# Optimization experiments

Hardware: AMD Instinct MI355X
Metric: run time of the kernel (lower is better)

## Reference

```python
import jax, jax.numpy as jnp
import numpy as np

N_NODES = 50000
N_EDGES = 800000
IN_DIM = 128
HIDDEN = 128
N_CLASSES = 10
BN_EPS = 1e-5


def _sage_conv(x, src, dst, n, w_l, b_l, w_r):
    # PyG SAGEConv (mean aggr): out = lin_l(mean_{j->i} x_j) + lin_r(x_i)
    msg = x[src]  # [E, d] gather
    s = jax.ops.segment_sum(msg, dst, num_segments=n)
    cnt = jax.ops.segment_sum(jnp.ones((src.shape[0], 1), x.dtype), dst, num_segments=n)
    mean = s / jnp.maximum(cnt, 1.0)
    return mean @ w_l.T + b_l + x @ w_r.T


def _bn_eval(x, gamma, beta, mean, var):
    return (x - mean) * (gamma * jax.lax.rsqrt(var + BN_EPS)) + beta


def setup_inputs() -> dict:
    key = jax.random.key(0)
    ks = jax.random.split(key, 16)
    h2 = HIDDEN // 2

    def lin(k, fan_out, fan_in):
        bound = 1.0 / np.sqrt(fan_in)
        return jax.random.uniform(k, (fan_out, fan_in), jnp.float32, -bound, bound)

    return {
        "x": jax.random.normal(ks[0], (N_NODES, IN_DIM), jnp.float32),
        "edge_index": jax.random.randint(ks[1], (2, N_EDGES), 0, N_NODES, jnp.int64),
        "w1l": lin(ks[2], HIDDEN, IN_DIM),
        "b1l": jnp.zeros((HIDDEN,), jnp.float32),
        "w1r": lin(ks[3], HIDDEN, IN_DIM),
        "bn1_gamma": jax.random.uniform(ks[4], (HIDDEN,), jnp.float32, 0.5, 1.5),
        "bn1_beta": jax.random.normal(ks[5], (HIDDEN,), jnp.float32) * 0.1,
        "bn1_mean": jax.random.normal(ks[6], (HIDDEN,), jnp.float32) * 0.1,
        "bn1_var": jax.random.uniform(ks[7], (HIDDEN,), jnp.float32, 0.5, 1.5),
        "w2l": lin(ks[8], h2, HIDDEN),
        "b2l": jnp.zeros((h2,), jnp.float32),
        "w2r": lin(ks[9], h2, HIDDEN),
        "bn2_gamma": jax.random.uniform(ks[10], (h2,), jnp.float32, 0.5, 1.5),
        "bn2_beta": jax.random.normal(ks[11], (h2,), jnp.float32) * 0.1,
        "bn2_mean": jax.random.normal(ks[12], (h2,), jnp.float32) * 0.1,
        "bn2_var": jax.random.uniform(ks[13], (h2,), jnp.float32, 0.5, 1.5),
        "head_w": lin(ks[14], N_CLASSES, h2),
        "head_b": jnp.zeros((N_CLASSES,), jnp.float32),
    }


def reference(x, edge_index, w1l, b1l, w1r, bn1_gamma, bn1_beta, bn1_mean, bn1_var,
              w2l, b2l, w2r, bn2_gamma, bn2_beta, bn2_mean, bn2_var, head_w, head_b):
    src, dst = edge_index[0], edge_index[1]
    n = x.shape[0]
    h = _sage_conv(x, src, dst, n, w1l, b1l, w1r)
    h = jax.nn.relu(_bn_eval(h, bn1_gamma, bn1_beta, bn1_mean, bn1_var))
    # dropout p=0.1 is identity in eval mode
    h = _sage_conv(h, src, dst, n, w2l, b2l, w2r)
    h = jax.nn.relu(_bn_eval(h, bn2_gamma, bn2_beta, bn2_mean, bn2_var))
    return h @ head_w.T + head_b
```

## Files before the change

### kernel.cpp

```cpp
#include <hip/hip_runtime.h>

typedef _Float16 f16;
typedef _Float16 f16x2 __attribute__((ext_vector_type(2)));
typedef _Float16 f16x4 __attribute__((ext_vector_type(4)));
typedef _Float16 f16x8 __attribute__((ext_vector_type(8)));
typedef float f32x4 __attribute__((ext_vector_type(4)));

#define N_NODES 50000
#define N_EDGES 800000
#define N_CLASSES 10
#define CAP 64
#define EDGE_BLOCKS ((N_EDGES + 255) / 256)

__global__ void zero_cnt_kernel(int* __restrict__ cnt) {
    int i = blockIdx.x * 256 + threadIdx.x;
    if (i < N_NODES / 4) ((int4*)cnt)[i] = make_int4(0, 0, 0, 0);
}

__global__ void build_fused_kernel(const int* __restrict__ src, const int* __restrict__ dst,
                                   int* __restrict__ cnt, unsigned short* __restrict__ bucket,
                                   const float* __restrict__ x,
                                   const float* __restrict__ w1l, const float* __restrict__ w1r,
                                   const float* __restrict__ w2l, const float* __restrict__ w2r,
                                   f16* __restrict__ xh, f16* __restrict__ W1, f16* __restrict__ W2cat) {
    int bid = blockIdx.x;
    if (bid < 2 * EDGE_BLOCKS) {
        int half = bid >> 1;
        if ((bid & 1) == 0) {
            int e = half * 256 + threadIdx.x;
            if (e < N_EDGES) {
                int d = dst[e];
                int s = atomicAdd(&cnt[d], 1);
                if (s < CAP) bucket[(long long)d * CAP + s] = (unsigned short)src[e];
            }
        } else {
            long long base = ((long long)half * 256 + threadIdx.x) * 8;
            float4 a = *(const float4*)(x + base);
            float4 b = *(const float4*)(x + base + 4);
            f16x8 o;
            o[0] = (f16)a.x; o[1] = (f16)a.y; o[2] = (f16)a.z; o[3] = (f16)a.w;
            o[4] = (f16)b.x; o[5] = (f16)b.y; o[6] = (f16)b.z; o[7] = (f16)b.w;
            *(f16x8*)(xh + base) = o;
        }
    } else {
        int wt = (bid - 2 * EDGE_BLOCKS) * 256 + threadIdx.x;
        for (int idx = wt; idx < 128 * 256; idx += 1024) {
            int n = idx >> 8, k = idx & 255;
            W1[idx] = (f16)(k < 128 ? w1l[n * 128 + k] : w1r[n * 128 + k - 128]);
        }
        for (int idx = wt; idx < 128 * 128; idx += 1024) {
            int n = idx >> 7, k = idx & 127;
            W2cat[idx] = (f16)(n < 64 ? w2l[n * 128 + k] : w2r[(n - 64) * 128 + k]);
        }
    }
}

__global__ void agg_mean_f16_kernel(const f16* __restrict__ feat,
                                    const int* __restrict__ cnt,
                                    const unsigned short* __restrict__ bucket,
                                    f16* __restrict__ outb) {
    int node = blockIdx.x * 8 + (threadIdx.x >> 5);
    int l  = threadIdx.x & 31;
    int bl = threadIdx.x & 32;
    int deg = cnt[node];
    int n_it = deg < CAP ? deg : CAP;
    const unsigned short* b = bucket + (long long)node * CAP;
    int my0 = (l < n_it)      ? (int)b[l]      : 0;
    int my1 = (32 + l < n_it) ? (int)b[32 + l] : 0;
    const f16x4* f4 = (const f16x4*)feat;
    float a0 = 0.f, a1 = 0.f, a2 = 0.f, a3 = 0.f;
    int j = 0;
    int lim0 = n_it < 32 ? n_it : 32;
    for (; j + 8 <= lim0; j += 8) {
        f16x4 v0 = f4[(long long)__shfl(my0, bl + j + 0) * 32 + l];
        f16x4 v1 = f4[(long long)__shfl(my0, bl + j + 1) * 32 + l];
        f16x4 v2 = f4[(long long)__shfl(my0, bl + j + 2) * 32 + l];
        f16x4 v3 = f4[(long long)__shfl(my0, bl + j + 3) * 32 + l];
        f16x4 v4 = f4[(long long)__shfl(my0, bl + j + 4) * 32 + l];
        f16x4 v5 = f4[(long long)__shfl(my0, bl + j + 5) * 32 + l];
        f16x4 v6 = f4[(long long)__shfl(my0, bl + j + 6) * 32 + l];
        f16x4 v7 = f4[(long long)__shfl(my0, bl + j + 7) * 32 + l];
        a0 += (((float)v0[0] + (float)v1[0]) + ((float)v2[0] + (float)v3[0]))
            + (((float)v4[0] + (float)v5[0]) + ((float)v6[0] + (float)v7[0]));
        a1 += (((float)v0[1] + (float)v1[1]) + ((float)v2[1] + (float)v3[1]))
            + (((float)v4[1] + (float)v5[1]) + ((float)v6[1] + (float)v7[1]));
        a2 += (((float)v0[2] + (float)v1[2]) + ((float)v2[2] + (float)v3[2]))
            + (((float)v4[2] + (float)v5[2]) + ((float)v6[2] + (float)v7[2]));
        a3 += (((float)v0[3] + (float)v1[3]) + ((float)v2[3] + (float)v3[3]))
            + (((float)v4[3] + (float)v5[3]) + ((float)v6[3] + (float)v7[3]));
    }
    for (; j < lim0; j++) {
        f16x4 v = f4[(long long)__shfl(my0, bl + j) * 32 + l];
        a0 += (float)v[0]; a1 += (float)v[1]; a2 += (float)v[2]; a3 += (float)v[3];
    }
    for (; j + 8 <= n_it; j += 8) {
        f16x4 v0 = f4[(long long)__shfl(my1, bl + j - 32 + 0) * 32 + l];
        f16x4 v1 = f4[(long long)__shfl(my1, bl + j - 32 + 1) * 32 + l];
        f16x4 v2 = f4[(long long)__shfl(my1, bl + j - 32 + 2) * 32 + l];
        f16x4 v3 = f4[(long long)__shfl(my1, bl + j - 32 + 3) * 32 + l];
        f16x4 v4 = f4[(long long)__shfl(my1, bl + j - 32 + 4) * 32 + l];
        f16x4 v5 = f4[(long long)__shfl(my1, bl + j - 32 + 5) * 32 + l];
        f16x4 v6 = f4[(long long)__shfl(my1, bl + j - 32 + 6) * 32 + l];
        f16x4 v7 = f4[(long long)__shfl(my1, bl + j - 32 + 7) * 32 + l];
        a0 += (((float)v0[0] + (float)v1[0]) + ((float)v2[0] + (float)v3[0]))
            + (((float)v4[0] + (float)v5[0]) + ((float)v6[0] + (float)v7[0]));
        a1 += (((float)v0[1] + (float)v1[1]) + ((float)v2[1] + (float)v3[1]))
            + (((float)v4[1] + (float)v5[1]) + ((float)v6[1] + (float)v7[1]));
        a2 += (((float)v0[2] + (float)v1[2]) + ((float)v2[2] + (float)v3[2]))
            + (((float)v4[2] + (float)v5[2]) + ((float)v6[2] + (float)v7[2]));
        a3 += (((float)v0[3] + (float)v1[3]) + ((float)v2[3] + (float)v3[3]))
            + (((float)v4[3] + (float)v5[3]) + ((float)v6[3] + (float)v7[3]));
    }
    for (; j < n_it; j++) {
        f16x4 v = f4[(long long)__shfl(my1, bl + j - 32) * 32 + l];
        a0 += (float)v[0]; a1 += (float)v[1]; a2 += (float)v[2]; a3 += (float)v[3];
    }
    float inv = 1.f / fmaxf((float)deg, 1.f);
    f16x4 r;
    r[0] = (f16)(a0 * inv); r[1] = (f16)(a1 * inv);
    r[2] = (f16)(a2 * inv); r[3] = (f16)(a3 * inv);
    ((f16x4*)outb)[(long long)node * 32 + l] = r;
}

__global__ __launch_bounds__(256) void sage1_kernel(
    const f16* __restrict__ Am, const f16* __restrict__ Ax,
    const f16* __restrict__ W1,
    const float* __restrict__ bias, const float* __restrict__ gamma,
    const float* __restrict__ beta, const float* __restrict__ bmean,
    const float* __restrict__ bvar, f16* __restrict__ C) {
    int tid  = threadIdx.x;
    int wave = tid >> 6;
    int lane = tid & 63;
    int m_base = blockIdx.x * 128 + wave * 32;
    int lrow = lane & 15;
    int lchunk = lane >> 4;

    f32x4 acc[2][8] = {};

#pragma unroll
    for (int phase = 0; phase < 2; phase++) {
        const f16* A = phase ? Ax : Am;
        const f16* Wp = W1 + phase * 128;
        f16x8 afrag[4][2];
#pragma unroll
        for (int kc = 0; kc < 4; kc++)
#pragma unroll
            for (int mf = 0; mf < 2; mf++) {
                int row = m_base + mf * 16 + lrow;
                row = row < N_NODES ? row : N_NODES - 1;
                afrag[kc][mf] = *(const f16x8*)(A + (long long)row * 128 + kc * 32 + lchunk * 8);
            }
#pragma unroll
        for (int nf = 0; nf < 8; nf++)
#pragma unroll
            for (int kc = 0; kc < 4; kc++) {
                f16x8 b = *(const f16x8*)(Wp + (long long)(nf * 16 + lrow) * 256
                                          + kc * 32 + lchunk * 8);
                acc[0][nf] = __builtin_amdgcn_mfma_f32_16x16x32_f16(afrag[kc][0], b, acc[0][nf], 0, 0, 0);
                acc[1][nf] = __builtin_amdgcn_mfma_f32_16x16x32_f16(afrag[kc][1], b, acc[1][nf], 0, 0, 0);
            }
    }

#pragma unroll
    for (int nf = 0; nf < 8; nf++) {
        int n = nf * 16 + lrow;
        float mul = gamma[n] * rsqrtf(bvar[n] + 1e-5f);
        float add = (bias[n] - bmean[n]) * mul + beta[n];
#pragma unroll
        for (int mf = 0; mf < 2; mf++)
#pragma unroll
            for (int r = 0; r < 4; r++) {
                int m = m_base + mf * 16 + lchunk * 4 + r;
                if (m < N_NODES) {
                    float v = fmaxf(fmaf(acc[mf][nf][r], mul, add), 0.f);
                    C[(long long)m * 128 + n] = (f16)v;
                }
            }
    }
}

__global__ __launch_bounds__(256) void y2_kernel(const f16* __restrict__ h1,
                                                 const f16* __restrict__ W2cat,
                                                 f16* __restrict__ y2) {
    int tid  = threadIdx.x;
    int wave = tid >> 6;
    int lane = tid & 63;
    int m_base = blockIdx.x * 128 + wave * 32;
    int lrow = lane & 15;
    int lchunk = lane >> 4;

    f16x8 afrag[4][2];
#pragma unroll
    for (int kc = 0; kc < 4; kc++)
#pragma unroll
        for (int mf = 0; mf < 2; mf++) {
            int row = m_base + mf * 16 + lrow;
            row = row < N_NODES ? row : N_NODES - 1;
            afrag[kc][mf] = *(const f16x8*)(h1 + (long long)row * 128 + kc * 32 + lchunk * 8);
        }

#pragma unroll
    for (int nf = 0; nf < 8; nf++) {
        f32x4 acc[2] = {};
#pragma unroll
        for (int kc = 0; kc < 4; kc++) {
            f16x8 b = *(const f16x8*)(W2cat + (long long)(nf * 16 + lrow) * 128
                                      + kc * 32 + lchunk * 8);
            acc[0] = __builtin_amdgcn_mfma_f32_16x16x32_f16(afrag[kc][0], b, acc[0], 0, 0, 0);
            acc[1] = __builtin_amdgcn_mfma_f32_16x16x32_f16(afrag[kc][1], b, acc[1], 0, 0, 0);
        }
        int n = nf * 16 + lrow;
#pragma unroll
        for (int mf = 0; mf < 2; mf++)
#pragma unroll
            for (int r = 0; r < 4; r++) {
                int m = m_base + mf * 16 + lchunk * 4 + r;
                if (m < N_NODES) y2[(long long)m * 128 + n] = (f16)acc[mf][r];
            }
    }
}

__global__ void agg_half_kernel(const f16* __restrict__ y2,
                                const int* __restrict__ cnt,
                                const unsigned short* __restrict__ bucket,
                                f16* __restrict__ mean2) {
    int node = blockIdx.x * 16 + (threadIdx.x >> 4);
    int l  = threadIdx.x & 15;
    int bl = threadIdx.x & 48;
    int deg = cnt[node];
    int n_it = deg < CAP ? deg : CAP;
    const unsigned short* b = bucket + (long long)node * CAP;
    int my0 = (l < n_it)      ? (int)b[l]      : 0;
    int my1 = (16 + l < n_it) ? (int)b[16 + l] : 0;
    int my2 = (32 + l < n_it) ? (int)b[32 + l] : 0;
    int my3 = (48 + l < n_it) ? (int)b[48 + l] : 0;
    const f16x4* f4 = (const f16x4*)y2;
    float a0 = 0.f, a1 = 0.f, a2 = 0.f, a3 = 0.f;
    int j = 0;

#define AGG_SEC(MYREG, BASE)                                                     \
    {                                                                            \
        int lim = n_it < (BASE + 16) ? n_it : (BASE + 16);                       \
        for (; j + 8 <= lim; j += 8) {                                           \
            f16x4 v0 = f4[(long long)__shfl(MYREG, bl + j - BASE + 0) * 32 + l]; \
            f16x4 v1 = f4[(long long)__shfl(MYREG, bl + j - BASE + 1) * 32 + l]; \
            f16x4 v2 = f4[(long long)__shfl(MYREG, bl + j - BASE + 2) * 32 + l]; \
            f16x4 v3 = f4[(long long)__shfl(MYREG, bl + j - BASE + 3) * 32 + l]; \
            f16x4 v4 = f4[(long long)__shfl(MYREG, bl + j - BASE + 4) * 32 + l]; \
            f16x4 v5 = f4[(long long)__shfl(MYREG, bl + j - BASE + 5) * 32 + l]; \
            f16x4 v6 = f4[(long long)__shfl(MYREG, bl + j - BASE + 6) * 32 + l]; \
            f16x4 v7 = f4[(long long)__shfl(MYREG, bl + j - BASE + 7) * 32 + l]; \
            a0 += (((float)v0[0] + (float)v1[0]) + ((float)v2[0] + (float)v3[0]))\
                + (((float)v4[0] + (float)v5[0]) + ((float)v6[0] + (float)v7[0]));\
            a1 += (((float)v0[1] + (float)v1[1]) + ((float)v2[1] + (float)v3[1]))\
                + (((float)v4[1] + (float)v5[1]) + ((float)v6[1] + (float)v7[1]));\
            a2 += (((float)v0[2] + (float)v1[2]) + ((float)v2[2] + (float)v3[2]))\
                + (((float)v4[2] + (float)v5[2]) + ((float)v6[2] + (float)v7[2]));\
            a3 += (((float)v0[3] + (float)v1[3]) + ((float)v2[3] + (float)v3[3]))\
                + (((float)v4[3] + (float)v5[3]) + ((float)v6[3] + (float)v7[3]));\
        }                                                                        \
        for (; j < lim; j++) {                                                   \
            f16x4 v = f4[(long long)__shfl(MYREG, bl + j - BASE) * 32 + l];      \
            a0 += (float)v[0]; a1 += (float)v[1];                                \
            a2 += (float)v[2]; a3 += (float)v[3];                                \
        }                                                                        \
    }

    AGG_SEC(my0, 0)
    AGG_SEC(my1, 16)
    AGG_SEC(my2, 32)
    AGG_SEC(my3, 48)
#undef AGG_SEC

    float inv = 1.f / fmaxf((float)deg, 1.f);
    f16x4 r;
    r[0] = (f16)(a0 * inv); r[1] = (f16)(a1 * inv);
    r[2] = (f16)(a2 * inv); r[3] = (f16)(a3 * inv);
    ((f16x4*)mean2)[(long long)node * 16 + l] = r;
}

__global__ void final_head_kernel(const f16* __restrict__ mean2,
                                  const f16* __restrict__ y2,
                                  const float* __restrict__ b2,
                                  const float* __restrict__ gamma,
                                  const float* __restrict__ beta,
                                  const float* __restrict__ bmean,
                                  const float* __restrict__ bvar,
                                  const float* __restrict__ hw,
                                  const float* __restrict__ hb,
                                  float* __restrict__ outp) {
    __shared__ f16 sm[128][68];
    int t = threadIdx.x;
    int rl = t >> 1, hh = t & 1;
    int m = blockIdx.x * 128 + rl;
    if (m < N_NODES) {
        int ch0 = hh * 32;
#pragma unroll
        for (int c = 0; c < 32; c += 8) {
            int ch = ch0 + c;
            f16x8 mv = *(const f16x8*)(mean2 + (long long)m * 64 + ch);
            f16x8 yv = *(const f16x8*)(y2 + (long long)m * 128 + 64 + ch);
#pragma unroll
            for (int i = 0; i < 8; i++) {
                int n = ch + i;
                float mul = gamma[n] * rsqrtf(bvar[n] + 1e-5f);
                float add = (b2[n] - bmean[n]) * mul + beta[n];
                float v = fmaf((float)mv[i] + (float)yv[i], mul, add);
                sm[rl][n] = (f16)fmaxf(v, 0.f);
            }
        }
    }
    __syncthreads();
    if (m < N_NODES) {
        int cb = hh * 5;
        float a0 = hb[cb + 0], a1 = hb[cb + 1], a2 = hb[cb + 2];
        float a3 = hb[cb + 3], a4 = hb[cb + 4];
#pragma unroll 8
        for (int k = 0; k < 64; k++) {
            float hv = (float)sm[rl][k];
            a0 = fmaf(hv, hw[(cb + 0) * 64 + k], a0);
            a1 = fmaf(hv, hw[(cb + 1) * 64 + k], a1);
            a2 = fmaf(hv, hw[(cb + 2) * 64 + k], a2);
            a3 = fmaf(hv, hw[(cb + 3) * 64 + k], a3);
            a4 = fmaf(hv, hw[(cb + 4) * 64 + k], a4);
        }
        float* op = outp + (long long)m * N_CLASSES + cb;
        op[0] = a0; op[1] = a1; op[2] = a2; op[3] = a3; op[4] = a4;
    }
}

extern "C" void kernel_launch(void* const* d_in, const int* in_sizes, int n_in,
                              void* d_out, int out_size, void* d_ws, size_t ws_size,
                              hipStream_t stream) {
    const float* x      = (const float*)d_in[0];
    const int*   ei     = (const int*)d_in[1];
    const float* w1l    = (const float*)d_in[2];
    const float* b1l    = (const float*)d_in[3];
    const float* w1r    = (const float*)d_in[4];
    const float* bn1_g  = (const float*)d_in[5];
    const float* bn1_b  = (const float*)d_in[6];
    const float* bn1_m  = (const float*)d_in[7];
    const float* bn1_v  = (const float*)d_in[8];
    const float* w2l    = (const float*)d_in[9];
    const float* b2l    = (const float*)d_in[10];
    const float* w2r    = (const float*)d_in[11];
    const float* bn2_g  = (const float*)d_in[12];
    const float* bn2_b  = (const float*)d_in[13];
    const float* bn2_m  = (const float*)d_in[14];
    const float* bn2_v  = (const float*)d_in[15];
    const float* head_w = (const float*)d_in[16];
    const float* head_b = (const float*)d_in[17];
    float* out = (float*)d_out;

    const int* src  = ei;
    const int* dstv = ei + N_EDGES;

    char* ws = (char*)d_ws;
    size_t off = 0;
    int* cnt               = (int*)(ws + off); off += ((size_t)N_NODES * 4 + 511) & ~511ull;
    unsigned short* bucket = (unsigned short*)(ws + off); off += (size_t)N_NODES * CAP * 2;
    f16* xh     = (f16*)(ws + off); off += (size_t)N_NODES * 128 * 2;
    f16* meanb  = (f16*)(ws + off); off += (size_t)N_NODES * 128 * 2;
    f16* h1     = (f16*)(ws + off); off += (size_t)N_NODES * 128 * 2;
    f16* y2     = (f16*)(ws + off); off += (size_t)N_NODES * 128 * 2;
    f16* mean2  = (f16*)(ws + off); off += (size_t)N_NODES * 64 * 2;
    f16* W1     = (f16*)(ws + off); off += (size_t)128 * 256 * 2;
    f16* W2cat  = (f16*)(ws + off); off += (size_t)128 * 128 * 2;

    zero_cnt_kernel<<<(N_NODES / 4 + 255) / 256, 256, 0, stream>>>(cnt);
    build_fused_kernel<<<2 * EDGE_BLOCKS + 4, 256, 0, stream>>>(
        src, dstv, cnt, bucket, x, w1l, w1r, w2l, w2r, xh, W1, W2cat);

    agg_mean_f16_kernel<<<N_NODES / 8, 256, 0, stream>>>(xh, cnt, bucket, meanb);
    sage1_kernel<<<(N_NODES + 127) / 128, 256, 0, stream>>>(
        meanb, xh, W1, b1l, bn1_g, bn1_b, bn1_m, bn1_v, h1);

    y2_kernel<<<(N_NODES + 127) / 128, 256, 0, stream>>>(h1, W2cat, y2);
    agg_half_kernel<<<N_NODES / 16, 256, 0, stream>>>(y2, cnt, bucket, mean2);
    final_head_kernel<<<(N_NODES + 127) / 128, 256, 0, stream>>>(
        mean2, y2, b2l, bn2_g, bn2_b, bn2_m, bn2_v, head_w, head_b, out);
}
```

Measured before the change: 155.2 us.

## Fuse layer-2 aggregation into head kernel and restructure build-kernel edge blocks

Merges the second-layer neighbor-mean kernel with the BN/ReLU/head kernel. Each block now aggregates its 128 nodes into shared memory, removing the mean2 round trip through global memory and one launch. Separately, the build kernel has each edge block process 4 edges per thread and gives the x-to-f16 conversion its own blocks, which cuts the edge-block count. In exchange, the fused kernel has fewer blocks (391) doing longer serial loops over 8 nodes per thread group, which may lower memory-level parallelism for the gather. Its inner unroll is also reduced from 8 to 4.

```diff
diff --git a/kernel.cpp b/kernel.cpp
--- a/kernel.cpp
+++ b/kernel.cpp
@@ -1,7 +1,6 @@
 #include <hip/hip_runtime.h>
 
 typedef _Float16 f16;
-typedef _Float16 f16x2 __attribute__((ext_vector_type(2)));
 typedef _Float16 f16x4 __attribute__((ext_vector_type(4)));
 typedef _Float16 f16x8 __attribute__((ext_vector_type(8)));
 typedef float f32x4 __attribute__((ext_vector_type(4)));
@@ -10,7 +9,8 @@
 #define N_EDGES 800000
 #define N_CLASSES 10
 #define CAP 64
-#define EDGE_BLOCKS ((N_EDGES + 255) / 256)
+#define EB4 ((N_EDGES + 1023) / 1024)
+#define XB  ((N_NODES * 128 / 8) / 256)
 
 __global__ void zero_cnt_kernel(int* __restrict__ cnt) {
     int i = blockIdx.x * 256 + threadIdx.x;
@@ -24,26 +24,27 @@
                                    const float* __restrict__ w2l, const float* __restrict__ w2r,
                                    f16* __restrict__ xh, f16* __restrict__ W1, f16* __restrict__ W2cat) {
     int bid = blockIdx.x;
-    if (bid < 2 * EDGE_BLOCKS) {
-        int half = bid >> 1;
-        if ((bid & 1) == 0) {
-            int e = half * 256 + threadIdx.x;
+    if (bid < EB4) {
+        int e0 = bid * 1024 + threadIdx.x;
+#pragma unroll
+        for (int q = 0; q < 4; q++) {
+            int e = e0 + q * 256;
             if (e < N_EDGES) {
                 int d = dst[e];
                 int s = atomicAdd(&cnt[d], 1);
                 if (s < CAP) bucket[(long long)d * CAP + s] = (unsigned short)src[e];
             }
-        } else {
-            long long base = ((long long)half * 256 + threadIdx.x) * 8;
-            float4 a = *(const float4*)(x + base);
-            float4 b = *(const float4*)(x + base + 4);
-            f16x8 o;
-            o[0] = (f16)a.x; o[1] = (f16)a.y; o[2] = (f16)a.z; o[3] = (f16)a.w;
-            o[4] = (f16)b.x; o[5] = (f16)b.y; o[6] = (f16)b.z; o[7] = (f16)b.w;
-            *(f16x8*)(xh + base) = o;
-        }
+        }
+    } else if (bid < EB4 + XB) {
+        long long base = ((long long)(bid - EB4) * 256 + threadIdx.x) * 8;
+        float4 a = *(const float4*)(x + base);
+        float4 b = *(const float4*)(x + base + 4);
+        f16x8 o;
+        o[0] = (f16)a.x; o[1] = (f16)a.y; o[2] = (f16)a.z; o[3] = (f16)a.w;
+        o[4] = (f16)b.x; o[5] = (f16)b.y; o[6] = (f16)b.z; o[7] = (f16)b.w;
+        *(f16x8*)(xh + base) = o;
     } else {
-        int wt = (bid - 2 * EDGE_BLOCKS) * 256 + threadIdx.x;
+        int wt = (bid - EB4 - XB) * 256 + threadIdx.x;
         for (int idx = wt; idx < 128 * 256; idx += 1024) {
             int n = idx >> 8, k = idx & 255;
             W1[idx] = (f16)(k < 128 ? w1l[n * 128 + k] : w1r[n * 128 + k - 128]);
@@ -220,97 +221,85 @@
     }
 }
 
-__global__ void agg_half_kernel(const f16* __restrict__ y2,
-                                const int* __restrict__ cnt,
-                                const unsigned short* __restrict__ bucket,
-                                f16* __restrict__ mean2) {
-    int node = blockIdx.x * 16 + (threadIdx.x >> 4);
-    int l  = threadIdx.x & 15;
-    int bl = threadIdx.x & 48;
-    int deg = cnt[node];
-    int n_it = deg < CAP ? deg : CAP;
-    const unsigned short* b = bucket + (long long)node * CAP;
-    int my0 = (l < n_it)      ? (int)b[l]      : 0;
-    int my1 = (16 + l < n_it) ? (int)b[16 + l] : 0;
-    int my2 = (32 + l < n_it) ? (int)b[32 + l] : 0;
-    int my3 = (48 + l < n_it) ? (int)b[48 + l] : 0;
-    const f16x4* f4 = (const f16x4*)y2;
-    float a0 = 0.f, a1 = 0.f, a2 = 0.f, a3 = 0.f;
-    int j = 0;
-
-#define AGG_SEC(MYREG, BASE)                                                     \
-    {                                                                            \
-        int lim = n_it < (BASE + 16) ? n_it : (BASE + 16);                       \
-        for (; j + 8 <= lim; j += 8) {                                           \
-            f16x4 v0 = f4[(long long)__shfl(MYREG, bl + j - BASE + 0) * 32 + l]; \
-            f16x4 v1 = f4[(long long)__shfl(MYREG, bl + j - BASE + 1) * 32 + l]; \
-            f16x4 v2 = f4[(long long)__shfl(MYREG, bl + j - BASE + 2) * 32 + l]; \
-            f16x4 v3 = f4[(long long)__shfl(MYREG, bl + j - BASE + 3) * 32 + l]; \
-            f16x4 v4 = f4[(long long)__shfl(MYREG, bl + j - BASE + 4) * 32 + l]; \
-            f16x4 v5 = f4[(long long)__shfl(MYREG, bl + j - BASE + 5) * 32 + l]; \
-            f16x4 v6 = f4[(long long)__shfl(MYREG, bl + j - BASE + 6) * 32 + l]; \
-            f16x4 v7 = f4[(long long)__shfl(MYREG, bl + j - BASE + 7) * 32 + l]; \
-            a0 += (((float)v0[0] + (float)v1[0]) + ((float)v2[0] + (float)v3[0]))\
-                + (((float)v4[0] + (float)v5[0]) + ((float)v6[0] + (float)v7[0]));\
-            a1 += (((float)v0[1] + (float)v1[1]) + ((float)v2[1] + (float)v3[1]))\
-                + (((float)v4[1] + (float)v5[1]) + ((float)v6[1] + (float)v7[1]));\
-            a2 += (((float)v0[2] + (float)v1[2]) + ((float)v2[2] + (float)v3[2]))\
-                + (((float)v4[2] + (float)v5[2]) + ((float)v6[2] + (float)v7[2]));\
-            a3 += (((float)v0[3] + (float)v1[3]) + ((float)v2[3] + (float)v3[3]))\
-                + (((float)v4[3] + (float)v5[3]) + ((float)v6[3] + (float)v7[3]));\
-        }                                                                        \
-        for (; j < lim; j++) {                                                   \
-            f16x4 v = f4[(long long)__shfl(MYREG, bl + j - BASE) * 32 + l];      \
-            a0 += (float)v[0]; a1 += (float)v[1];                                \
-            a2 += (float)v[2]; a3 += (float)v[3];                                \
-        }                                                                        \
-    }
-
-    AGG_SEC(my0, 0)
-    AGG_SEC(my1, 16)
-    AGG_SEC(my2, 32)
-    AGG_SEC(my3, 48)
-#undef AGG_SEC
-
-    float inv = 1.f / fmaxf((float)deg, 1.f);
-    f16x4 r;
-    r[0] = (f16)(a0 * inv); r[1] = (f16)(a1 * inv);
-    r[2] = (f16)(a2 * inv); r[3] = (f16)(a3 * inv);
-    ((f16x4*)mean2)[(long long)node * 16 + l] = r;
-}
-
-__global__ void final_head_kernel(const f16* __restrict__ mean2,
-                                  const f16* __restrict__ y2,
-                                  const float* __restrict__ b2,
-                                  const float* __restrict__ gamma,
-                                  const float* __restrict__ beta,
-                                  const float* __restrict__ bmean,
-                                  const float* __restrict__ bvar,
-                                  const float* __restrict__ hw,
-                                  const float* __restrict__ hb,
-                                  float* __restrict__ outp) {
+__global__ __launch_bounds__(256) void agg_final_kernel(
+    const f16* __restrict__ y2,
+    const int* __restrict__ cnt,
+    const unsigned short* __restrict__ bucket,
+    const float* __restrict__ b2,
+    const float* __restrict__ gamma,
+    const float* __restrict__ beta,
+    const float* __restrict__ bmean,
+    const float* __restrict__ bvar,
+    const float* __restrict__ hw,
+    const float* __restrict__ hb,
+    float* __restrict__ outp) {
     __shared__ f16 sm[128][68];
     int t = threadIdx.x;
+    int l  = t & 15;
+    int bl = t & 48;
+    int grp = t >> 4;
+
+    float mul4[4], add4[4];
+#pragma unroll
+    for (int i = 0; i < 4; i++) {
+        int n = l * 4 + i;
+        mul4[i] = gamma[n] * rsqrtf(bvar[n] + 1e-5f);
+        add4[i] = (b2[n] - bmean[n]) * mul4[i] + beta[n];
+    }
+
+    const f16x4* f4 = (const f16x4*)y2;
+
+    for (int it = 0; it < 8; it++) {
+        int nloc = it * 16 + grp;
+        int node = blockIdx.x * 128 + nloc;
+        if (node < N_NODES) {
+            int deg = cnt[node];
+            int n_it = deg < CAP ? deg : CAP;
+            const unsigned short* b = bucket + (long long)node * CAP;
+            int my0 = (l < n_it)      ? (int)b[l]      : 0;
+            int my1 = (16 + l < n_it) ? (int)b[16 + l] : 0;
+            int my2 = (32 + l < n_it) ? (int)b[32 + l] : 0;
+            int my3 = (48 + l < n_it) ? (int)b[48 + l] : 0;
+            float a0 = 0.f, a1 = 0.f, a2 = 0.f, a3 = 0.f;
+            int j = 0;
+#define AGG_SEC(MYREG, BASE)                                                     \
+            {                                                                    \
+                int lim = n_it < (BASE + 16) ? n_it : (BASE + 16);               \
+                for (; j + 4 <= lim; j += 4) {                                   \
+                    f16x4 v0 = f4[(long long)__shfl(MYREG, bl + j - BASE + 0) * 32 + l]; \
+                    f16x4 v1 = f4[(long long)__shfl(MYREG, bl + j - BASE + 1) * 32 + l]; \
+                    f16x4 v2 = f4[(long long)__shfl(MYREG, bl + j - BASE + 2) * 32 + l]; \
+                    f16x4 v3 = f4[(long long)__shfl(MYREG, bl + j - BASE + 3) * 32 + l]; \
+                    a0 += ((float)v0[0] + (float)v1[0]) + ((float)v2[0] + (float)v3[0]); \
+                    a1 += ((float)v0[1] + (float)v1[1]) + ((float)v2[1] + (float)v3[1]); \
+                    a2 += ((float)v0[2] + (float)v1[2]) + ((float)v2[2] + (float)v3[2]); \
+                    a3 += ((float)v0[3] + (float)v1[3]) + ((float)v2[3] + (float)v3[3]); \
+                }                                                                \
+                for (; j < lim; j++) {                                           \
+                    f16x4 v = f4[(long long)__shfl(MYREG, bl + j - BASE) * 32 + l]; \
+                    a0 += (float)v[0]; a1 += (float)v[1];                        \
+                    a2 += (float)v[2]; a3 += (float)v[3];                        \
+                }                                                                \
+            }
+            AGG_SEC(my0, 0)
+            AGG_SEC(my1, 16)
+            AGG_SEC(my2, 32)
+            AGG_SEC(my3, 48)
+#undef AGG_SEC
+            float inv = 1.f / fmaxf((float)deg, 1.f);
+            f16x4 yr = f4[(long long)node * 32 + 16 + l];
+            f16x4 r;
+            r[0] = (f16)fmaxf(fmaf(a0 * inv + (float)yr[0], mul4[0], add4[0]), 0.f);
+            r[1] = (f16)fmaxf(fmaf(a1 * inv + (float)yr[1], mul4[1], add4[1]), 0.f);
+            r[2] = (f16)fmaxf(fmaf(a2 * inv + (float)yr[2], mul4[2], add4[2]), 0.f);
+            r[3] = (f16)fmaxf(fmaf(a3 * inv + (float)yr[3], mul4[3], add4[3]), 0.f);
+            *(f16x4*)&sm[nloc][l * 4] = r;
+        }
+    }
+    __syncthreads();
+
     int rl = t >> 1, hh = t & 1;
     int m = blockIdx.x * 128 + rl;
-    if (m < N_NODES) {
-        int ch0 = hh * 32;
-#pragma unroll
-        for (int c = 0; c < 32; c += 8) {
-            int ch = ch0 + c;
-            f16x8 mv = *(const f16x8*)(mean2 + (long long)m * 64 + ch);
-            f16x8 yv = *(const f16x8*)(y2 + (long long)m * 128 + 64 + ch);
-#pragma unroll
-            for (int i = 0; i < 8; i++) {
-                int n = ch + i;
-                float mul = gamma[n] * rsqrtf(bvar[n] + 1e-5f);
-                float add = (b2[n] - bmean[n]) * mul + beta[n];
-                float v = fmaf((float)mv[i] + (float)yv[i], mul, add);
-                sm[rl][n] = (f16)fmaxf(v, 0.f);
-            }
-        }
-    }
-    __syncthreads();
     if (m < N_NODES) {
         int cb = hh * 5;
         float a0 = hb[cb + 0], a1 = hb[cb + 1], a2 = hb[cb + 2];
@@ -363,12 +352,11 @@
     f16* meanb  = (f16*)(ws + off); off += (size_t)N_NODES * 128 * 2;
     f16* h1     = (f16*)(ws + off); off += (size_t)N_NODES * 128 * 2;
     f16* y2     = (f16*)(ws + off); off += (size_t)N_NODES * 128 * 2;
-    f16* mean2  = (f16*)(ws + off); off += (size_t)N_NODES * 64 * 2;
     f16* W1     = (f16*)(ws + off); off += (size_t)128 * 256 * 2;
     f16* W2cat  = (f16*)(ws + off); off += (size_t)128 * 128 * 2;
 
     zero_cnt_kernel<<<(N_NODES / 4 + 255) / 256, 256, 0, stream>>>(cnt);
-    build_fused_kernel<<<2 * EDGE_BLOCKS + 4, 256, 0, stream>>>(
+    build_fused_kernel<<<EB4 + XB + 4, 256, 0, stream>>>(
         src, dstv, cnt, bucket, x, w1l, w1r, w2l, w2r, xh, W1, W2cat);
 
     agg_mean_f16_kernel<<<N_NODES / 8, 256, 0, stream>>>(xh, cnt, bucket, meanb);
@@ -376,7 +364,6 @@
         meanb, xh, W1, b1l, bn1_g, bn1_b, bn1_m, bn1_v, h1);
 
     y2_kernel<<<(N_NODES + 127) / 128, 256, 0, stream>>>(h1, W2cat, y2);
-    agg_half_kernel<<<N_NODES / 16, 256, 0, stream>>>(y2, cnt, bucket, mean2);
-    final_head_kernel<<<(N_NODES + 127) / 128, 256, 0, stream>>>(
-        mean2, y2, b2l, bn2_g, bn2_b, bn2_m, bn2_v, head_w, head_b, out);
-}
+    agg_final_kernel<<<(N_NODES + 127) / 128, 256, 0, stream>>>(
+        y2, cnt, bucket, b2l, bn2_g, bn2_b, bn2_m, bn2_v, head_w, head_b, out);
+}
```

New measurement: 176.8 us. +13.9%, slower.
